# Kernel tuning notes

Hardware: AMD Instinct MI355X
Metric: run time of the kernel (lower is better)

The kernel has to match this reference:

```python
import jax, jax.numpy as jnp
import numpy as np

N, D, H, C = 50000, 128, 4, 16  # nodes, in_dim, heads, out per head
E, ED = 800000, 64              # edges, edge feature dim
NEG_SLOPE = 0.2


def setup_inputs() -> dict:
    key = jax.random.key(0)
    ks = jax.random.split(key, 10)
    x = jax.random.normal(ks[0], (N, D), dtype=jnp.float32)
    edge_index = jax.random.randint(ks[1], (2, E), 0, N, dtype=jnp.int64)
    edge_attr = jax.random.normal(ks[2], (E, ED), dtype=jnp.float32)
    s = 0.1
    W = jax.random.normal(ks[3], (H * C, D), dtype=jnp.float32) * s       # lin (no bias)
    W_edge = jax.random.normal(ks[4], (H * C, ED), dtype=jnp.float32) * s  # lin_edge (no bias)
    att_src = jax.random.normal(ks[5], (H, C), dtype=jnp.float32) * s
    att_dst = jax.random.normal(ks[6], (H, C), dtype=jnp.float32) * s
    att_edge = jax.random.normal(ks[7], (H, C), dtype=jnp.float32) * s
    bias = jnp.zeros((H * C,), dtype=jnp.float32)
    return dict(x=x, edge_index=edge_index, edge_attr=edge_attr, W=W,
                W_edge=W_edge, att_src=att_src, att_dst=att_dst,
                att_edge=att_edge, bias=bias)


def reference(x, edge_index, edge_attr, W, W_edge, att_src, att_dst, att_edge, bias):
    n = x.shape[0]
    src0, dst0 = edge_index[0], edge_index[1]

    # PyG GATConv default: add self-loops, self-loop edge_attr = per-dst mean of incoming edge_attr
    ones = jnp.ones((src0.shape[0],), dtype=edge_attr.dtype)
    cnt = jax.ops.segment_sum(ones, dst0, num_segments=n)                # [N]
    loop_attr = jax.ops.segment_sum(edge_attr, dst0, num_segments=n)
    loop_attr = loop_attr / jnp.maximum(cnt, 1.0)[:, None]               # [N, ED]
    ar = jnp.arange(n, dtype=src0.dtype)
    src = jnp.concatenate([src0, ar])
    dst = jnp.concatenate([dst0, ar])
    ea = jnp.concatenate([edge_attr, loop_attr], axis=0)                 # [E+N, ED]

    xh = (x @ W.T).reshape(n, H, C)                                      # [N, H, C]
    a_src = jnp.einsum('nhc,hc->nh', xh, att_src)                        # [N, H]
    a_dst = jnp.einsum('nhc,hc->nh', xh, att_dst)
    eh = (ea @ W_edge.T).reshape(-1, H, C)                               # [E+N, H, C]
    a_edge = jnp.einsum('ehc,hc->eh', eh, att_edge)                      # [E+N, H]

    alpha = a_src[src] + a_dst[dst] + a_edge                             # [E+N, H]
    alpha = jax.nn.leaky_relu(alpha, NEG_SLOPE)

    # softmax over edges grouped by destination node (PyG softmax)
    amax = jax.ops.segment_max(alpha, dst, num_segments=n)               # [N, H]
    alpha = jnp.exp(alpha - amax[dst])
    denom = jax.ops.segment_sum(alpha, dst, num_segments=n)
    alpha = alpha / (denom[dst] + 1e-16)

    # message = x_j * alpha, scatter-add to destination
    out = jax.ops.segment_sum(xh[src] * alpha[:, :, None], dst, num_segments=n)  # [N,H,C]
    return out.reshape(n, H * C) + bias
```

## Files before the change

### kernel.cpp

```cpp
#include <hip/hip_runtime.h>
#include <math.h>

#define N_NODES 50000
#define DIM     128
#define NHEAD   4
#define NCH     16
#define HC      64
#define NE      800000
#define EDIM    64
#define NEG     0.2f
#define MAXE    64

__device__ __forceinline__ float lrelu(float v) { return v > 0.f ? v : NEG * v; }

__global__ __launch_bounds__(256) void k2_xh(const float* __restrict__ x, const float* __restrict__ W,
                                             const float* __restrict__ att_src, const float* __restrict__ att_dst,
                                             float* __restrict__ xh, float* __restrict__ a_src,
                                             float* __restrict__ a_dst) {
    __shared__ float Wt[128 * 68];
    int t = threadIdx.x;
    for (int idx = t; idx < 64 * 128; idx += 256) {
        int col = idx >> 7, k = idx & 127;
        Wt[k * 68 + col] = W[idx];
    }
    __syncthreads();

    int h  = t & 3;
    int rp = t >> 2;
    int row0 = blockIdx.x * 128 + rp * 2;
    int r0 = min(row0, N_NODES - 1);
    int r1 = min(row0 + 1, N_NODES - 1);
    const float4* x0 = (const float4*)(x + (size_t)r0 * DIM);
    const float4* x1 = (const float4*)(x + (size_t)r1 * DIM);

    float acc0[16], acc1[16];
    #pragma unroll
    for (int c = 0; c < 16; ++c) { acc0[c] = 0.f; acc1[c] = 0.f; }

    for (int k4 = 0; k4 < 32; ++k4) {
        float4 xa = x0[k4];
        float4 xb = x1[k4];
        #pragma unroll
        for (int kk = 0; kk < 4; ++kk) {
            float va = (&xa.x)[kk];
            float vb = (&xb.x)[kk];
            const float* wr = &Wt[(k4 * 4 + kk) * 68 + h * 16];
            #pragma unroll
            for (int j = 0; j < 4; ++j) {
                float4 w = *(const float4*)(wr + 4 * j);
                acc0[4 * j + 0] = fmaf(va, w.x, acc0[4 * j + 0]);
                acc0[4 * j + 1] = fmaf(va, w.y, acc0[4 * j + 1]);
                acc0[4 * j + 2] = fmaf(va, w.z, acc0[4 * j + 2]);
                acc0[4 * j + 3] = fmaf(va, w.w, acc0[4 * j + 3]);
                acc1[4 * j + 0] = fmaf(vb, w.x, acc1[4 * j + 0]);
                acc1[4 * j + 1] = fmaf(vb, w.y, acc1[4 * j + 1]);
                acc1[4 * j + 2] = fmaf(vb, w.z, acc1[4 * j + 2]);
                acc1[4 * j + 3] = fmaf(vb, w.w, acc1[4 * j + 3]);
            }
        }
    }

    if (row0 < N_NODES) {
        float4* o = (float4*)(xh + (size_t)row0 * HC + h * 16);
        o[0] = make_float4(acc0[0], acc0[1], acc0[2], acc0[3]);
        o[1] = make_float4(acc0[4], acc0[5], acc0[6], acc0[7]);
        o[2] = make_float4(acc0[8], acc0[9], acc0[10], acc0[11]);
        o[3] = make_float4(acc0[12], acc0[13], acc0[14], acc0[15]);
        float ss = 0.f, sd = 0.f;
        #pragma unroll
        for (int c = 0; c < 16; ++c) {
            ss = fmaf(acc0[c], att_src[h * 16 + c], ss);
            sd = fmaf(acc0[c], att_dst[h * 16 + c], sd);
        }
        a_src[row0 * 4 + h] = ss;
        a_dst[row0 * 4 + h] = sd;
    }
    if (row0 + 1 < N_NODES) {
        float4* o = (float4*)(xh + (size_t)(row0 + 1) * HC + h * 16);
        o[0] = make_float4(acc1[0], acc1[1], acc1[2], acc1[3]);
        o[1] = make_float4(acc1[4], acc1[5], acc1[6], acc1[7]);
        o[2] = make_float4(acc1[8], acc1[9], acc1[10], acc1[11]);
        o[3] = make_float4(acc1[12], acc1[13], acc1[14], acc1[15]);
        float ss = 0.f, sd = 0.f;
        #pragma unroll
        for (int c = 0; c < 16; ++c) {
            ss = fmaf(acc1[c], att_src[h * 16 + c], ss);
            sd = fmaf(acc1[c], att_dst[h * 16 + c], sd);
        }
        a_src[(row0 + 1) * 4 + h] = ss;
        a_dst[(row0 + 1) * 4 + h] = sd;
    }
}

__global__ __launch_bounds__(256) void ka_deg(const int* __restrict__ ei, int* __restrict__ deg,
                                              int* __restrict__ rank) {
    int e = blockIdx.x * 256 + threadIdx.x;
    if (e >= NE) return;
    rank[e] = atomicAdd(deg + ei[NE + e], 1);
}

__global__ void k4a_scan(const int* __restrict__ deg, int* __restrict__ tmp, int* __restrict__ bsums) {
    int t = threadIdx.x;
    int i = blockIdx.x * 256 + t;
    int v = (i < N_NODES) ? deg[i] : 0;
    int lane = t & 63, w = t >> 6;
    int xv = v;
    #pragma unroll
    for (int o = 1; o < 64; o <<= 1) {
        int y = __shfl_up(xv, o);
        if (lane >= o) xv += y;
    }
    __shared__ int wtot[4];
    if (lane == 63) wtot[w] = xv;
    __syncthreads();
    int add = 0;
    #pragma unroll
    for (int j = 0; j < 4; ++j)
        if (j < w) add += wtot[j];
    xv += add;
    if (i < N_NODES) tmp[i] = xv;
    if (t == 255) bsums[blockIdx.x] = xv;
}

__global__ void k4b_scan(int* __restrict__ bsums, int nb) {
    int t = threadIdx.x;
    int v = (t < nb) ? bsums[t] : 0;
    int lane = t & 63, w = t >> 6;
    int xv = v;
    #pragma unroll
    for (int o = 1; o < 64; o <<= 1) {
        int y = __shfl_up(xv, o);
        if (lane >= o) xv += y;
    }
    __shared__ int wtot[4];
    if (lane == 63) wtot[w] = xv;
    __syncthreads();
    int add = 0;
    #pragma unroll
    for (int j = 0; j < 4; ++j)
        if (j < w) add += wtot[j];
    xv += add;
    if (t < nb) bsums[t] = xv - v;
}

__global__ void k4c_finish(const int* __restrict__ tmp, const int* __restrict__ bsums,
                           int* __restrict__ rowptr) {
    int i = blockIdx.x * 256 + threadIdx.x;
    if (i >= N_NODES) return;
    int incl = tmp[i] + bsums[i >> 8];
    rowptr[i + 1] = incl;
    if (i == 0) rowptr[0] = 0;
}

__global__ __launch_bounds__(256) void kp_csr2(const float* __restrict__ edge_attr,
                                               const float* __restrict__ W_edge,
                                               const float* __restrict__ att_edge,
                                               const int* __restrict__ ei,
                                               const int* __restrict__ rank,
                                               const int* __restrict__ rowptr,
                                               int* __restrict__ csr_src,
                                               float* __restrict__ csr_p) {
    __shared__ __align__(16) float sv[256];
    int t = threadIdx.x;
    {
        int h = t >> 6, d = t & 63;
        float acc = 0.f;
        #pragma unroll
        for (int c = 0; c < NCH; ++c)
            acc = fmaf(att_edge[h * NCH + c], W_edge[(h * NCH + c) * EDIM + d], acc);
        sv[h * 64 + d] = acc;
    }
    __syncthreads();

    int lane = t & 63;
    int q = lane & 15;
    float4 w0 = *(const float4*)(sv + 0 * 64 + q * 4);
    float4 w1 = *(const float4*)(sv + 1 * 64 + q * 4);
    float4 w2 = *(const float4*)(sv + 2 * 64 + q * 4);
    float4 w3 = *(const float4*)(sv + 3 * 64 + q * 4);

    int wave   = (blockIdx.x * 256 + t) >> 6;
    int nwaves = gridDim.x * 4;
    for (int g = wave; g < NE / 4; g += nwaves) {
        int src = 0, pos = 0;
        if (q == 0) {
            int e = g * 4 + (lane >> 4);
            src = ei[e];
            int dst = ei[NE + e];
            pos = rowptr[dst] + rank[e];
        }
        float4 v = *(const float4*)(edge_attr + (size_t)g * 256 + lane * 4);
        float p0 = fmaf(v.x, w0.x, fmaf(v.y, w0.y, fmaf(v.z, w0.z, v.w * w0.w)));
        float p1 = fmaf(v.x, w1.x, fmaf(v.y, w1.y, fmaf(v.z, w1.z, v.w * w1.w)));
        float p2 = fmaf(v.x, w2.x, fmaf(v.y, w2.y, fmaf(v.z, w2.z, v.w * w2.w)));
        float p3 = fmaf(v.x, w3.x, fmaf(v.y, w3.y, fmaf(v.z, w3.z, v.w * w3.w)));
        #pragma unroll
        for (int m = 1; m < 16; m <<= 1) {
            p0 += __shfl_xor(p0, m);
            p1 += __shfl_xor(p1, m);
            p2 += __shfl_xor(p2, m);
            p3 += __shfl_xor(p3, m);
        }
        if (q == 0) {
            csr_src[pos] = src;
            *(float4*)(csr_p + (size_t)pos * 4) = make_float4(p0, p1, p2, p3);
        }
    }
}

__global__ __launch_bounds__(256) void k6_agg(const int* __restrict__ rowptr,
                                              const int* __restrict__ csr_src,
                                              const float* __restrict__ csr_p,
                                              const float* __restrict__ xh,
                                              const float* __restrict__ a_src,
                                              const float* __restrict__ a_dst,
                                              const float* __restrict__ bias,
                                              float* __restrict__ out) {
    __shared__ __align__(16) float s_w[4][MAXE][4];
    __shared__ int s_src[4][MAXE];
    int wid  = threadIdx.x >> 6;
    int lane = threadIdx.x & 63;
    int n = blockIdx.x * 4 + wid;
    int start = rowptr[n], end = rowptr[n + 1];
    int degn = end - start;
    int m = min(degn, MAXE);

    for (int i = lane; i < m; i += 64) {
        s_src[wid][i] = csr_src[start + i];
        *(float4*)&s_w[wid][i][0] = *(const float4*)(csr_p + (size_t)(start + i) * 4);
    }
    __syncthreads();

    int h = lane & 3;
    float adh = a_dst[n * 4 + h];
    float sw = 0.f, sp = 0.f;
    for (int i = lane >> 2; i < m; i += 16) {
        int s   = s_src[wid][i];
        float p = s_w[wid][i][h];
        float w = __expf(lrelu(a_src[(size_t)s * 4 + h] + adh + p));
        s_w[wid][i][h] = w;
        sw += w;
        sp += p;
    }
    for (int i = MAXE + (lane >> 2); i < degn; i += 16) {
        int s = csr_src[start + i];
        float p = csr_p[(size_t)(start + i) * 4 + h];
        sw += __expf(lrelu(a_src[(size_t)s * 4 + h] + adh + p));
        sp += p;
    }
    sw += __shfl_xor(sw, 4);  sp += __shfl_xor(sp, 4);
    sw += __shfl_xor(sw, 8);  sp += __shfl_xor(sp, 8);
    sw += __shfl_xor(sw, 16); sp += __shfl_xor(sp, 16);
    sw += __shfl_xor(sw, 32); sp += __shfl_xor(sp, 32);

    float al    = sp / fmaxf((float)degn, 1.f);
    float wself = __expf(lrelu(a_src[n * 4 + h] + adh + al));
    float denom = sw + wself + 1e-16f;
    __syncthreads();

    int h2 = lane >> 4;
    float d2   = __shfl(denom, h2);
    float ws2  = __shfl(wself, h2);
    float adh2 = __shfl(adh, h2);
    float acc = ws2 * xh[(size_t)n * HC + lane];

    int i = 0;
    for (; i + 4 <= m; i += 4) {
        int s0 = s_src[wid][i], s1 = s_src[wid][i + 1];
        int s2 = s_src[wid][i + 2], s3 = s_src[wid][i + 3];
        float w0 = s_w[wid][i][h2],     w1 = s_w[wid][i + 1][h2];
        float w2 = s_w[wid][i + 2][h2], w3 = s_w[wid][i + 3][h2];
        float x0 = xh[(size_t)s0 * HC + lane];
        float x1 = xh[(size_t)s1 * HC + lane];
        float x2 = xh[(size_t)s2 * HC + lane];
        float x3 = xh[(size_t)s3 * HC + lane];
        acc = fmaf(w0, x0, acc);
        acc = fmaf(w1, x1, acc);
        acc = fmaf(w2, x2, acc);
        acc = fmaf(w3, x3, acc);
    }
    for (; i < m; ++i) {
        int s = s_src[wid][i];
        acc = fmaf(s_w[wid][i][h2], xh[(size_t)s * HC + lane], acc);
    }
    for (int j = MAXE; j < degn; ++j) {
        int s = csr_src[start + j];
        float p = csr_p[(size_t)(start + j) * 4 + h2];
        float w = __expf(lrelu(a_src[(size_t)s * 4 + h2] + adh2 + p));
        acc = fmaf(w, xh[(size_t)s * HC + lane], acc);
    }
    out[(size_t)n * HC + lane] = acc / d2 + bias[lane];
}

extern "C" void kernel_launch(void* const* d_in, const int* in_sizes, int n_in,
                              void* d_out, int out_size, void* d_ws, size_t ws_size,
                              hipStream_t stream) {
    const float* x         = (const float*)d_in[0];
    const int*   ei        = (const int*)d_in[1];
    const float* edge_attr = (const float*)d_in[2];
    const float* W         = (const float*)d_in[3];
    const float* W_edge    = (const float*)d_in[4];
    const float* att_src   = (const float*)d_in[5];
    const float* att_dst   = (const float*)d_in[6];
    const float* att_edge  = (const float*)d_in[7];
    const float* bias      = (const float*)d_in[8];
    float* out = (float*)d_out;

    char* ws = (char*)d_ws;
    size_t off = 0;
    float* xh        = (float*)(ws + off); off += (size_t)N_NODES * HC * 4;
    float* a_src     = (float*)(ws + off); off += (size_t)N_NODES * 4 * 4;
    float* a_dst     = (float*)(ws + off); off += (size_t)N_NODES * 4 * 4;
    int*   deg       = (int*)(ws + off);   off += (size_t)N_NODES * 4;
    int*   tmp       = (int*)(ws + off);   off += (size_t)N_NODES * 4;
    int*   bsums     = (int*)(ws + off);   off += 1024;
    int*   rowptr    = (int*)(ws + off);   off += (size_t)(N_NODES + 4) * 4;
    int*   rank      = (int*)(ws + off);   off += (size_t)NE * 4;
    int*   csr_src   = (int*)(ws + off);   off += (size_t)NE * 4;
    float* csr_p     = (float*)(ws + off); off += (size_t)NE * 4 * 4;

    hipMemsetAsync(deg, 0, (size_t)N_NODES * 4, stream);

    k2_xh<<<(N_NODES + 127) / 128, 256, 0, stream>>>(x, W, att_src, att_dst, xh, a_src, a_dst);
    ka_deg<<<(NE + 255) / 256, 256, 0, stream>>>(ei, deg, rank);
    int nb = (N_NODES + 255) / 256;
    k4a_scan<<<nb, 256, 0, stream>>>(deg, tmp, bsums);
    k4b_scan<<<1, 256, 0, stream>>>(bsums, nb);
    k4c_finish<<<nb, 256, 0, stream>>>(tmp, bsums, rowptr);
    kp_csr2<<<2048, 256, 0, stream>>>(edge_attr, W_edge, att_edge, ei, rank, rowptr,
                                      csr_src, csr_p);
    k6_agg<<<N_NODES / 4, 256, 0, stream>>>(rowptr, csr_src, csr_p, xh,
                                            a_src, a_dst, bias, out);
}
```

Measured before the change: 432.5 us.

## Split CSR build into permutation scatter and gather-side edge projection

Replaces the single kernel that read edge_attr in order and scattered src and per-head scores to CSR positions with two kernels. The first writes a permutation of edge ids into CSR order. The second walks CSR order, gathers edge_attr rows and src indices through the permutation, computes the four-head projections (two edges per 16-lane group), and writes csr_src and csr_p contiguously. The aim is to trade scattered small writes for coalesced writes. The cost is an extra launch, an extra permutation buffer, and random 256-byte row reads of edge_attr plus random src lookups.

```diff
diff --git a/kernel.cpp b/kernel.cpp
--- a/kernel.cpp
+++ b/kernel.cpp
@@ -152,14 +152,23 @@
     if (i == 0) rowptr[0] = 0;
 }
 
-__global__ __launch_bounds__(256) void kp_csr2(const float* __restrict__ edge_attr,
-                                               const float* __restrict__ W_edge,
-                                               const float* __restrict__ att_edge,
-                                               const int* __restrict__ ei,
+__global__ __launch_bounds__(256) void kp_perm(const int* __restrict__ ei,
                                                const int* __restrict__ rank,
                                                const int* __restrict__ rowptr,
-                                               int* __restrict__ csr_src,
-                                               float* __restrict__ csr_p) {
+                                               int* __restrict__ perm) {
+    int e = blockIdx.x * 256 + threadIdx.x;
+    if (e >= NE) return;
+    int dst = ei[NE + e];
+    perm[rowptr[dst] + rank[e]] = e;
+}
+
+__global__ __launch_bounds__(256) void kp_gather(const int* __restrict__ perm,
+                                                 const int* __restrict__ ei,
+                                                 const float* __restrict__ edge_attr,
+                                                 const float* __restrict__ W_edge,
+                                                 const float* __restrict__ att_edge,
+                                                 int* __restrict__ csr_src,
+                                                 float* __restrict__ csr_p) {
     __shared__ __align__(16) float sv[256];
     int t = threadIdx.x;
     {
@@ -173,7 +182,8 @@
     __syncthreads();
 
     int lane = t & 63;
-    int q = lane & 15;
+    int sub  = lane >> 4;
+    int q    = lane & 15;
     float4 w0 = *(const float4*)(sv + 0 * 64 + q * 4);
     float4 w1 = *(const float4*)(sv + 1 * 64 + q * 4);
     float4 w2 = *(const float4*)(sv + 2 * 64 + q * 4);
@@ -181,29 +191,34 @@
 
     int wave   = (blockIdx.x * 256 + t) >> 6;
     int nwaves = gridDim.x * 4;
-    for (int g = wave; g < NE / 4; g += nwaves) {
-        int src = 0, pos = 0;
+    const int NP = NE / 8;
+    for (int gp = wave; gp < NP; gp += nwaves) {
+        int i0 = gp * 8 + sub;
+        int i1 = i0 + 4;
+        int e0 = perm[i0];
+        int e1 = perm[i1];
+        float4 va = *(const float4*)(edge_attr + (size_t)e0 * EDIM + q * 4);
+        float4 vb = *(const float4*)(edge_attr + (size_t)e1 * EDIM + q * 4);
+        float a0 = fmaf(va.x, w0.x, fmaf(va.y, w0.y, fmaf(va.z, w0.z, va.w * w0.w)));
+        float a1 = fmaf(va.x, w1.x, fmaf(va.y, w1.y, fmaf(va.z, w1.z, va.w * w1.w)));
+        float a2 = fmaf(va.x, w2.x, fmaf(va.y, w2.y, fmaf(va.z, w2.z, va.w * w2.w)));
+        float a3 = fmaf(va.x, w3.x, fmaf(va.y, w3.y, fmaf(va.z, w3.z, va.w * w3.w)));
+        float b0 = fmaf(vb.x, w0.x, fmaf(vb.y, w0.y, fmaf(vb.z, w0.z, vb.w * w0.w)));
+        float b1 = fmaf(vb.x, w1.x, fmaf(vb.y, w1.y, fmaf(vb.z, w1.z, vb.w * w1.w)));
+        float b2 = fmaf(vb.x, w2.x, fmaf(vb.y, w2.y, fmaf(vb.z, w2.z, vb.w * w2.w)));
+        float b3 = fmaf(vb.x, w3.x, fmaf(vb.y, w3.y, fmaf(vb.z, w3.z, vb.w * w3.w)));
+        #pragma unroll
+        for (int mm = 1; mm < 16; mm <<= 1) {
+            a0 += __shfl_xor(a0, mm); a1 += __shfl_xor(a1, mm);
+            a2 += __shfl_xor(a2, mm); a3 += __shfl_xor(a3, mm);
+            b0 += __shfl_xor(b0, mm); b1 += __shfl_xor(b1, mm);
+            b2 += __shfl_xor(b2, mm); b3 += __shfl_xor(b3, mm);
+        }
         if (q == 0) {
-            int e = g * 4 + (lane >> 4);
-            src = ei[e];
-            int dst = ei[NE + e];
-            pos = rowptr[dst] + rank[e];
-        }
-        float4 v = *(const float4*)(edge_attr + (size_t)g * 256 + lane * 4);
-        float p0 = fmaf(v.x, w0.x, fmaf(v.y, w0.y, fmaf(v.z, w0.z, v.w * w0.w)));
-        float p1 = fmaf(v.x, w1.x, fmaf(v.y, w1.y, fmaf(v.z, w1.z, v.w * w1.w)));
-        float p2 = fmaf(v.x, w2.x, fmaf(v.y, w2.y, fmaf(v.z, w2.z, v.w * w2.w)));
-        float p3 = fmaf(v.x, w3.x, fmaf(v.y, w3.y, fmaf(v.z, w3.z, v.w * w3.w)));
-        #pragma unroll
-        for (int m = 1; m < 16; m <<= 1) {
-            p0 += __shfl_xor(p0, m);
-            p1 += __shfl_xor(p1, m);
-            p2 += __shfl_xor(p2, m);
-            p3 += __shfl_xor(p3, m);
-        }
-        if (q == 0) {
-            csr_src[pos] = src;
-            *(float4*)(csr_p + (size_t)pos * 4) = make_float4(p0, p1, p2, p3);
+            csr_src[i0] = ei[e0];
+            csr_src[i1] = ei[e1];
+            *(float4*)(csr_p + (size_t)i0 * 4) = make_float4(a0, a1, a2, a3);
+            *(float4*)(csr_p + (size_t)i1 * 4) = make_float4(b0, b1, b2, b3);
         }
     }
 }
@@ -316,6 +331,7 @@
     int*   bsums     = (int*)(ws + off);   off += 1024;
     int*   rowptr    = (int*)(ws + off);   off += (size_t)(N_NODES + 4) * 4;
     int*   rank      = (int*)(ws + off);   off += (size_t)NE * 4;
+    int*   perm      = (int*)(ws + off);   off += (size_t)NE * 4;
     int*   csr_src   = (int*)(ws + off);   off += (size_t)NE * 4;
     float* csr_p     = (float*)(ws + off); off += (size_t)NE * 4 * 4;
 
@@ -327,8 +343,9 @@
     k4a_scan<<<nb, 256, 0, stream>>>(deg, tmp, bsums);
     k4b_scan<<<1, 256, 0, stream>>>(bsums, nb);
     k4c_finish<<<nb, 256, 0, stream>>>(tmp, bsums, rowptr);
-    kp_csr2<<<2048, 256, 0, stream>>>(edge_attr, W_edge, att_edge, ei, rank, rowptr,
-                                      csr_src, csr_p);
+    kp_perm<<<(NE + 255) / 256, 256, 0, stream>>>(ei, rank, rowptr, perm);
+    kp_gather<<<2048, 256, 0, stream>>>(perm, ei, edge_attr, W_edge, att_edge,
+                                        csr_src, csr_p);
     k6_agg<<<N_NODES / 4, 256, 0, stream>>>(rowptr, csr_src, csr_p, xh,
                                             a_src, a_dst, bias, out);
 }
```

After: 440.6 us. No clear change (+1.9%).
